# Optimization experiments

Measured on AMD Instinct MI355X. Metric: run time of the kernel, lower is better.

## Reference

```python
import jax, jax.numpy as jnp
import numpy as np

D_MODEL = 4096
NUM_HEADS = 64
DEPTH = D_MODEL // NUM_HEADS  # 64
B = 64   # must equal NUM_HEADS (quirk of original rope-after-split-heads code)
S = 64   # must equal NUM_HEADS (S*DEPTH must equal D_MODEL)


def setup_inputs() -> dict:
    key = jax.random.key(0)
    ks = jax.random.split(key, 9)
    scale = 1.0 / np.sqrt(D_MODEL)
    d = {"x": jax.random.normal(ks[0], (B, S, D_MODEL), dtype=jnp.float32)}
    for i, n in enumerate(["q", "k", "v", "o"]):
        d[f"w_{n}"] = jax.random.normal(ks[1 + i], (D_MODEL, D_MODEL), dtype=jnp.float32) * scale
        d[f"b_{n}"] = jax.random.normal(ks[5 + i], (D_MODEL,), dtype=jnp.float32) * 0.01
    return d


def _rope(x):
    # Faithful to the original: rope is applied to (B, H, S, depth) and treats
    # dim 1 (heads) as the 'sequence' axis, with inv_freq sized for full d_model.
    inv_freq = 1.0 / (10000.0 ** (jnp.arange(0, D_MODEL, 2, dtype=jnp.float32) / D_MODEL))
    pos = jnp.arange(x.shape[1], dtype=jnp.float32)[:, None]       # (H, 1)
    sinusoid = pos * inv_freq                                       # (H, d_model/2)
    sin = jnp.sin(sinusoid)[None, :, None, :]                       # (1, H, 1, d_model/2)
    cos = jnp.cos(sinusoid)[None, :, None, :]
    xr = x.reshape(x.shape[0], x.shape[1], -1, 2)                   # (B, H, S*depth/2, 2)
    real, imag = xr[..., 0], xr[..., 1]                             # (B, H, M) with M == d_model/2
    rot_real = real * cos - imag * sin                              # broadcasts to (1, B, H, M)
    rot_imag = real * sin + imag * cos
    return jnp.stack((rot_real, rot_imag), axis=-1).reshape(x.shape)


def reference(x, w_q, b_q, w_k, b_k, w_v, b_v, w_o, b_o):
    def split_heads(t):  # (B, S, d_model) -> (B, H, S, depth)
        return t.reshape(B, S, NUM_HEADS, DEPTH).transpose(0, 2, 1, 3)

    q = split_heads(x @ w_q.T + b_q)
    k = split_heads(x @ w_k.T + b_k)
    v = split_heads(x @ w_v.T + b_v)
    q = _rope(q)
    k = _rope(k)

    scores = jnp.einsum("bhqd,bhkd->bhqk", q, k) / np.sqrt(DEPTH).astype(np.float32)
    weights = jax.nn.softmax(scores, axis=-1)
    out = jnp.einsum("bhqk,bhkd->bhqd", weights, v)
    out = out.transpose(0, 2, 1, 3).reshape(B, S, D_MODEL)
    return out @ w_o.T + b_o
```

## Files before the change

kernel.cpp:

```cpp
#include <hip/hip_runtime.h>
#include <cstdint>
#include <cstddef>


typedef _Float16 half8 __attribute__((ext_vector_type(8)));
typedef float floatx4 __attribute__((ext_vector_type(4)));

#define D_MODEL 4096
#define ROWS    4096
#define NEG_LOG2_10000_OVER_2048 (-0.0064881408103278559f)

__device__ __forceinline__ void gl_lds16(const void* g, void* l) {
    __builtin_amdgcn_global_load_lds(
        (const __attribute__((address_space(1))) void*)(void*)g,
        (__attribute__((address_space(3))) void*)l,
        16, 0, 0);
}

__global__ __launch_bounds__(256) void cast_f16_kernel(
    const float* __restrict__ s, _Float16* __restrict__ d, int n)
{
    int i0 = (blockIdx.x * 256 + threadIdx.x) * 8;
    int stride = gridDim.x * 256 * 8;
    for (int i = i0; i < n; i += stride) {
        const float4 a = *(const float4*)(s + i);
        const float4 b = *(const float4*)(s + i + 4);
        half8 h;
        h[0] = (_Float16)a.x; h[1] = (_Float16)a.y;
        h[2] = (_Float16)a.z; h[3] = (_Float16)a.w;
        h[4] = (_Float16)b.x; h[5] = (_Float16)b.y;
        h[6] = (_Float16)b.z; h[7] = (_Float16)b.w;
        *(half8*)(d + i) = h;
    }
}

template <int OUT_F16>
__global__ __launch_bounds__(256, 2) void gemm_nt_kernel(
    const _Float16* __restrict__ A, const _Float16* __restrict__ B,
    const float* __restrict__ bias, void* __restrict__ Cout,
    int M, int N, int K)
{
    __shared__ __align__(16) _Float16 As[128 * 32];
    __shared__ __align__(16) _Float16 Bs[128 * 32];

    const int tid  = threadIdx.x;
    const int col0 = blockIdx.x * 128;
    const int row0 = blockIdx.y * 128;
    const int wave = tid >> 6;
    const int lane = tid & 63;
    const int wm = (wave >> 1) * 64;
    const int wn = (wave & 1) * 64;

    floatx4 zero = {0.f, 0.f, 0.f, 0.f};
    floatx4 acc[4][4];
#pragma unroll
    for (int i = 0; i < 4; i++)
#pragma unroll
        for (int j = 0; j < 4; j++) acc[i][j] = zero;

    const int ar = tid >> 2;
    const int ac = (tid & 3) * 8;
    const _Float16* Ag0 = A + (size_t)(row0 + ar) * K + ac;
    const _Float16* Ag1 = A + (size_t)(row0 + 64 + ar) * K + ac;
    const _Float16* Bg0 = B + (size_t)(col0 + ar) * K + ac;
    const _Float16* Bg1 = B + (size_t)(col0 + 64 + ar) * K + ac;
    _Float16* As0 = As + tid * 8;
    _Float16* As1 = As + (tid + 256) * 8;
    _Float16* Bs0 = Bs + tid * 8;
    _Float16* Bs1 = Bs + (tid + 256) * 8;

    const int fr = lane & 15;
    const int fc = (lane >> 4) * 8;

    for (int kt = 0; kt < K; kt += 32) {
        gl_lds16(Ag0 + kt, As0);
        gl_lds16(Ag1 + kt, As1);
        gl_lds16(Bg0 + kt, Bs0);
        gl_lds16(Bg1 + kt, Bs1);
        __syncthreads();

        half8 af[4], bf[4];
#pragma unroll
        for (int t = 0; t < 4; t++) {
            af[t] = *(const half8*)(As + (size_t)(wm + t * 16 + fr) * 32 + fc);
            bf[t] = *(const half8*)(Bs + (size_t)(wn + t * 16 + fr) * 32 + fc);
        }
#pragma unroll
        for (int i = 0; i < 4; i++)
#pragma unroll
            for (int j = 0; j < 4; j++)
                acc[i][j] = __builtin_amdgcn_mfma_f32_16x16x32_f16(
                    af[i], bf[j], acc[i][j], 0, 0, 0);
        __syncthreads();
    }

    const int crow = row0 + wm + ((lane >> 4) << 2);
    const int ccol = col0 + wn + (lane & 15);
#pragma unroll
    for (int i = 0; i < 4; i++) {
#pragma unroll
        for (int j = 0; j < 4; j++) {
            const int gc = ccol + j * 16;
            const float bv = bias[gc];
#pragma unroll
            for (int r2 = 0; r2 < 4; r2++) {
                const int gr = crow + i * 16 + r2;
                const float v = acc[i][j][r2] + bv;
                if (OUT_F16)
                    ((_Float16*)Cout)[(size_t)gr * N + gc] = (_Float16)v;
                else
                    ((float*)Cout)[(size_t)gr * N + gc] = v;
            }
        }
    }
}

__global__ __launch_bounds__(256) void attn_kernel(
    const _Float16* __restrict__ qkv, _Float16* __restrict__ out)
{
    __shared__ __align__(16) _Float16 qs[64][72];
    __shared__ __align__(16) _Float16 ks[64][72];
    __shared__ __align__(16) _Float16 vt[64][72];
    __shared__ __align__(16) _Float16 ps[4][16][72];

    const int tid  = threadIdx.x;
    const int bb   = blockIdx.x >> 6;
    const int hh   = blockIdx.x & 63;
    const int wave = tid >> 6;
    const int lane = tid & 63;
    const int r  = tid >> 2;
    const int cb = (tid & 3) * 8;
    const float fb = (float)bb;

    const _Float16* grow = qkv + (size_t)(bb * 64 + r) * 12288 + hh * 64;

#pragma unroll
    for (int u = 0; u < 2; u++) {
        const int c8 = cb + u * 32;
        half8 q8 = *(const half8*)(grow + c8);
        half8 k8 = *(const half8*)(grow + 4096 + c8);
        half8 v8 = *(const half8*)(grow + 8192 + c8);
#pragma unroll
        for (int p = 0; p < 4; p++) {
            const int m = r * 32 + (c8 >> 1) + p;
            const float theta = fb * exp2f((float)m * NEG_LOG2_10000_OVER_2048);
            float sn, cs;
            __sincosf(theta, &sn, &cs);
            const float qe = (float)q8[2 * p], qo = (float)q8[2 * p + 1];
            q8[2 * p]     = (_Float16)(qe * cs - qo * sn);
            q8[2 * p + 1] = (_Float16)(qe * sn + qo * cs);
            const float ke = (float)k8[2 * p], ko = (float)k8[2 * p + 1];
            k8[2 * p]     = (_Float16)(ke * cs - ko * sn);
            k8[2 * p + 1] = (_Float16)(ke * sn + ko * cs);
        }
        *(half8*)&qs[r][c8] = q8;
        *(half8*)&ks[r][c8] = k8;
#pragma unroll
        for (int j = 0; j < 8; j++) vt[c8 + j][r] = v8[j];
    }
    __syncthreads();

    const int fr = lane & 15;
    const int fc = (lane >> 4) * 8;

    floatx4 sa[4];
#pragma unroll
    for (int t = 0; t < 4; t++) sa[t] = (floatx4){0.f, 0.f, 0.f, 0.f};
    half8 a0 = *(const half8*)&qs[wave * 16 + fr][fc];
    half8 a1 = *(const half8*)&qs[wave * 16 + fr][fc + 32];
#pragma unroll
    for (int t = 0; t < 4; t++) {
        half8 kb0 = *(const half8*)&ks[t * 16 + fr][fc];
        half8 kb1 = *(const half8*)&ks[t * 16 + fr][fc + 32];
        sa[t] = __builtin_amdgcn_mfma_f32_16x16x32_f16(a0, kb0, sa[t], 0, 0, 0);
        sa[t] = __builtin_amdgcn_mfma_f32_16x16x32_f16(a1, kb1, sa[t], 0, 0, 0);
    }

#pragma unroll
    for (int i = 0; i < 4; i++) {
        float mx = -1e30f;
#pragma unroll
        for (int t = 0; t < 4; t++) mx = fmaxf(mx, sa[t][i]);
#pragma unroll
        for (int d = 1; d < 16; d <<= 1) mx = fmaxf(mx, __shfl_xor(mx, d));
        float sum = 0.f;
        float pv[4];
#pragma unroll
        for (int t = 0; t < 4; t++) {
            const float e = __expf((sa[t][i] - mx) * 0.125f);
            pv[t] = e;
            sum += e;
        }
#pragma unroll
        for (int d = 1; d < 16; d <<= 1) sum += __shfl_xor(sum, d);
        const float inv = 1.0f / sum;
        const int prow = ((lane >> 4) << 2) + i;
#pragma unroll
        for (int t = 0; t < 4; t++)
            ps[wave][prow][t * 16 + fr] = (_Float16)(pv[t] * inv);
    }

    half8 pa0 = *(const half8*)&ps[wave][fr][fc];
    half8 pa1 = *(const half8*)&ps[wave][fr][fc + 32];
    floatx4 oa[4];
#pragma unroll
    for (int t = 0; t < 4; t++) oa[t] = (floatx4){0.f, 0.f, 0.f, 0.f};
#pragma unroll
    for (int t = 0; t < 4; t++) {
        half8 vb0 = *(const half8*)&vt[t * 16 + fr][fc];
        half8 vb1 = *(const half8*)&vt[t * 16 + fr][fc + 32];
        oa[t] = __builtin_amdgcn_mfma_f32_16x16x32_f16(pa0, vb0, oa[t], 0, 0, 0);
        oa[t] = __builtin_amdgcn_mfma_f32_16x16x32_f16(pa1, vb1, oa[t], 0, 0, 0);
    }

    _Float16* obase = out + (size_t)(bb * 64) * 4096 + hh * 64;
#pragma unroll
    for (int t = 0; t < 4; t++)
#pragma unroll
        for (int i = 0; i < 4; i++) {
            const int sq = wave * 16 + ((lane >> 4) << 2) + i;
            obase[(size_t)sq * 4096 + t * 16 + fr] = (_Float16)oa[t][i];
        }
}

extern "C" void kernel_launch(void* const* d_in, const int* in_sizes, int n_in,
                              void* d_out, int out_size, void* d_ws, size_t ws_size,
                              hipStream_t stream)
{
    const float* x  = (const float*)d_in[0];
    const float* wq = (const float*)d_in[1];
    const float* bq = (const float*)d_in[2];
    const float* wk = (const float*)d_in[3];
    const float* bk = (const float*)d_in[4];
    const float* wv = (const float*)d_in[5];
    const float* bv = (const float*)d_in[6];
    const float* wo = (const float*)d_in[7];
    const float* bo = (const float*)d_in[8];

    const size_t NELT = (size_t)4096 * 4096;
    char* ws = (char*)d_ws;
    _Float16* xh      = (_Float16*)(ws);
    _Float16* wcat    = (_Float16*)(ws + 33554432);
    _Float16* woh     = (_Float16*)(ws + 134217728);
    _Float16* qkv     = (_Float16*)(ws + 167772160);
    _Float16* attnbuf = (_Float16*)(ws + 268435456);
    float*    biascat = (float*)(ws + 301989888);

    const dim3 cg(1024), cb(256);
    cast_f16_kernel<<<cg, cb, 0, stream>>>(x,  xh,              (int)NELT);
    cast_f16_kernel<<<cg, cb, 0, stream>>>(wq, wcat,            (int)NELT);
    cast_f16_kernel<<<cg, cb, 0, stream>>>(wk, wcat + NELT,     (int)NELT);
    cast_f16_kernel<<<cg, cb, 0, stream>>>(wv, wcat + 2 * NELT, (int)NELT);
    cast_f16_kernel<<<cg, cb, 0, stream>>>(wo, woh,             (int)NELT);
    hipMemcpyAsync(biascat,        bq, 4096 * sizeof(float), hipMemcpyDeviceToDevice, stream);
    hipMemcpyAsync(biascat + 4096, bk, 4096 * sizeof(float), hipMemcpyDeviceToDevice, stream);
    hipMemcpyAsync(biascat + 8192, bv, 4096 * sizeof(float), hipMemcpyDeviceToDevice, stream);

    gemm_nt_kernel<1><<<dim3(96, 32), dim3(256), 0, stream>>>(
        xh, wcat, biascat, qkv, 4096, 12288, 4096);

    attn_kernel<<<dim3(4096), dim3(256), 0, stream>>>(qkv, attnbuf);

    gemm_nt_kernel<0><<<dim3(32, 32), dim3(256), 0, stream>>>(
        attnbuf, woh, bo, d_out, 4096, 4096, 4096);
}
```

Measured before the change: 1.007 ms.

## Swizzle GEMM LDS layout and merge cast and bias-copy launches

Applies an XOR/rotation-style swizzle to the k-chunk position of each row in the GEMM shared-memory tiles, on both the global-to-LDS load and the fragment reads. The goal is to remove LDS bank conflicts when the waves read their half8 fragments. It also folds five fp32-to-fp16 cast launches into one 2D-grid kernel and replaces three device memcpys with a small bias-concatenation kernel, cutting launch overhead. The swizzle adds index arithmetic, and the load and read mappings must agree exactly.

```diff
diff --git a/kernel.cpp b/kernel.cpp
--- a/kernel.cpp
+++ b/kernel.cpp
@@ -6,8 +6,7 @@
 typedef _Float16 half8 __attribute__((ext_vector_type(8)));
 typedef float floatx4 __attribute__((ext_vector_type(4)));
 
-#define D_MODEL 4096
-#define ROWS    4096
+#define NELT_W 16777216u
 #define NEG_LOG2_10000_OVER_2048 (-0.0064881408103278559f)
 
 __device__ __forceinline__ void gl_lds16(const void* g, void* l) {
@@ -17,12 +16,25 @@
         16, 0, 0);
 }
 
-__global__ __launch_bounds__(256) void cast_f16_kernel(
-    const float* __restrict__ s, _Float16* __restrict__ d, int n)
-{
+__global__ __launch_bounds__(256) void cast5_kernel(
+    const float* __restrict__ x,  const float* __restrict__ wq,
+    const float* __restrict__ wk, const float* __restrict__ wv,
+    const float* __restrict__ wo,
+    _Float16* __restrict__ xh, _Float16* __restrict__ wcat,
+    _Float16* __restrict__ woh)
+{
+    const float* s;
+    _Float16* d;
+    switch (blockIdx.y) {
+        case 0:  s = x;  d = xh;                 break;
+        case 1:  s = wq; d = wcat;               break;
+        case 2:  s = wk; d = wcat + NELT_W;      break;
+        case 3:  s = wv; d = wcat + 2 * NELT_W;  break;
+        default: s = wo; d = woh;                break;
+    }
     int i0 = (blockIdx.x * 256 + threadIdx.x) * 8;
     int stride = gridDim.x * 256 * 8;
-    for (int i = i0; i < n; i += stride) {
+    for (int i = i0; i < (int)NELT_W; i += stride) {
         const float4 a = *(const float4*)(s + i);
         const float4 b = *(const float4*)(s + i + 4);
         half8 h;
@@ -34,6 +46,18 @@
     }
 }
 
+__global__ __launch_bounds__(256) void biascat_kernel(
+    const float* __restrict__ bq, const float* __restrict__ bk,
+    const float* __restrict__ bv, float* __restrict__ out)
+{
+    int i = blockIdx.x * 256 + threadIdx.x;
+    if (i < 4096) {
+        out[i]        = bq[i];
+        out[4096 + i] = bk[i];
+        out[8192 + i] = bv[i];
+    }
+}
+
 template <int OUT_F16>
 __global__ __launch_bounds__(256, 2) void gemm_nt_kernel(
     const _Float16* __restrict__ A, const _Float16* __restrict__ B,
@@ -59,7 +83,7 @@
         for (int j = 0; j < 4; j++) acc[i][j] = zero;
 
     const int ar = tid >> 2;
-    const int ac = (tid & 3) * 8;
+    const int ac = (((tid & 3) - (ar >> 1)) & 3) * 8;
     const _Float16* Ag0 = A + (size_t)(row0 + ar) * K + ac;
     const _Float16* Ag1 = A + (size_t)(row0 + 64 + ar) * K + ac;
     const _Float16* Bg0 = B + (size_t)(col0 + ar) * K + ac;
@@ -70,7 +94,7 @@
     _Float16* Bs1 = Bs + (tid + 256) * 8;
 
     const int fr = lane & 15;
-    const int fc = (lane >> 4) * 8;
+    const int kc = lane >> 4;
 
     for (int kt = 0; kt < K; kt += 32) {
         gl_lds16(Ag0 + kt, As0);
@@ -82,8 +106,12 @@
         half8 af[4], bf[4];
 #pragma unroll
         for (int t = 0; t < 4; t++) {
-            af[t] = *(const half8*)(As + (size_t)(wm + t * 16 + fr) * 32 + fc);
-            bf[t] = *(const half8*)(Bs + (size_t)(wn + t * 16 + fr) * 32 + fc);
+            const int rowa = wm + t * 16 + fr;
+            const int rowb = wn + t * 16 + fr;
+            const int pa = ((kc + (rowa >> 1)) & 3) * 8;
+            const int pb = ((kc + (rowb >> 1)) & 3) * 8;
+            af[t] = *(const half8*)(As + (size_t)rowa * 32 + pa);
+            bf[t] = *(const half8*)(Bs + (size_t)rowb * 32 + pb);
         }
 #pragma unroll
         for (int i = 0; i < 4; i++)
@@ -246,15 +274,9 @@
     _Float16* attnbuf = (_Float16*)(ws + 268435456);
     float*    biascat = (float*)(ws + 301989888);
 
-    const dim3 cg(1024), cb(256);
-    cast_f16_kernel<<<cg, cb, 0, stream>>>(x,  xh,              (int)NELT);
-    cast_f16_kernel<<<cg, cb, 0, stream>>>(wq, wcat,            (int)NELT);
-    cast_f16_kernel<<<cg, cb, 0, stream>>>(wk, wcat + NELT,     (int)NELT);
-    cast_f16_kernel<<<cg, cb, 0, stream>>>(wv, wcat + 2 * NELT, (int)NELT);
-    cast_f16_kernel<<<cg, cb, 0, stream>>>(wo, woh,             (int)NELT);
-    hipMemcpyAsync(biascat,        bq, 4096 * sizeof(float), hipMemcpyDeviceToDevice, stream);
-    hipMemcpyAsync(biascat + 4096, bk, 4096 * sizeof(float), hipMemcpyDeviceToDevice, stream);
-    hipMemcpyAsync(biascat + 8192, bv, 4096 * sizeof(float), hipMemcpyDeviceToDevice, stream);
+    cast5_kernel<<<dim3(1024, 5), dim3(256), 0, stream>>>(
+        x, wq, wk, wv, wo, xh, wcat, woh);
+    biascat_kernel<<<dim3(16), dim3(256), 0, stream>>>(bq, bk, bv, biascat);
 
     gemm_nt_kernel<1><<<dim3(96, 32), dim3(256), 0, stream>>>(
         xh, wcat, biascat, qkv, 4096, 12288, 4096);
```

Measured after the change: 1.003 ms. Within noise of the previous version (-0.4%).
